# Performance work log

Measured on AMD Instinct MI355X. Metric: run time of the kernel, lower is better.

Reference implementation:

```python
import jax, jax.numpy as jnp
import numpy as np

N_NODES = 50000


def _pointnet_layer(h, pos, src, dst, wA, bA, wB, bB):
    # message: MLP(concat(h_j, pos_j - pos_i)) per edge, then max-aggregate at dst
    m = jnp.concatenate([h[src], pos[src] - pos[dst]], axis=-1)  # [E, in+3]
    m = jax.nn.relu(m @ wA + bA) @ wB + bB                       # [E, out]
    agg = jax.ops.segment_max(m, dst, num_segments=N_NODES)     # [N, out]
    # PyG max-aggregation returns 0 for nodes with no incoming edges
    return jnp.where(jnp.isfinite(agg), agg, 0.0)


def setup_inputs() -> dict:
    key = jax.random.key(0)
    ks = jax.random.split(key, 16)
    num_points, num_features, E = 256, 256, 800000
    s = 0.05
    inp = {
        "x": jax.random.normal(ks[0], (N_NODES, num_points), dtype=jnp.float32),
        "pos": jax.random.normal(ks[1], (N_NODES, 3), dtype=jnp.float32),
        "edge_index": jax.random.randint(ks[2], (2, E), 0, N_NODES, dtype=jnp.int64),
        # conv1 mlp: (num_points+3 -> F -> F)
        "w1a": jax.random.normal(ks[3], (num_points + 3, num_features), dtype=jnp.float32) * s,
        "b1a": jnp.zeros((num_features,), dtype=jnp.float32),
        "w1b": jax.random.normal(ks[4], (num_features, num_features), dtype=jnp.float32) * s,
        "b1b": jnp.zeros((num_features,), dtype=jnp.float32),
        # conv2 mlp: (F+3 -> F -> F)
        "w2a": jax.random.normal(ks[5], (num_features + 3, num_features), dtype=jnp.float32) * s,
        "b2a": jnp.zeros((num_features,), dtype=jnp.float32),
        "w2b": jax.random.normal(ks[6], (num_features, num_features), dtype=jnp.float32) * s,
        "b2b": jnp.zeros((num_features,), dtype=jnp.float32),
        # decoder: F -> 256 -> num_points
        "wd1": jax.random.normal(ks[7], (num_features, 256), dtype=jnp.float32) * s,
        "bd1": jnp.zeros((256,), dtype=jnp.float32),
        "wd2": jax.random.normal(ks[8], (256, num_points), dtype=jnp.float32) * s,
        "bd2": jnp.zeros((num_points,), dtype=jnp.float32),
    }
    return inp


def reference(x, pos, edge_index, w1a, b1a, w1b, b1b, w2a, b2a, w2b, b2b, wd1, bd1, wd2, bd2):
    src, dst = edge_index[0], edge_index[1]  # message flows j(src) -> i(dst)
    h = jax.nn.relu(_pointnet_layer(x, pos, src, dst, w1a, b1a, w1b, b1b))
    h = jax.nn.relu(_pointnet_layer(h, pos, src, dst, w2a, b2a, w2b, b2b))
    decoded = jax.nn.relu(h @ wd1 + bd1) @ wd2 + bd2  # [N, num_points]
    return decoded
```

## Files before the change

### kernel.cpp

```cpp
#include <hip/hip_runtime.h>
#include <stdint.h>


using bf16x8 = __attribute__((ext_vector_type(8))) short;
using f32x4  = __attribute__((ext_vector_type(4))) float;

#define AB_STRIDE 40
#define ZSTRIDE   68

__device__ __forceinline__ float b2f(uint32_t v16) {
    return __uint_as_float(v16 << 16);
}
__device__ __forceinline__ float b2f_hi(uint32_t w) {
    return __uint_as_float(w & 0xffff0000u);
}
__device__ __forceinline__ uint16_t f2b(float f) {
    uint32_t u = __float_as_uint(f);
    u += 0x7fffu + ((u >> 16) & 1u);
    return (uint16_t)(u >> 16);
}
#if __has_builtin(__builtin_amdgcn_cvt_pk_bf16_f32)
__device__ __forceinline__ uint32_t pack2bf(float lo, float hi) {
    auto r = __builtin_amdgcn_cvt_pk_bf16_f32(lo, hi);
    uint32_t u; __builtin_memcpy(&u, &r, 4); return u;
}
#else
__device__ __forceinline__ uint32_t pack2bf(float lo, float hi) {
    return (uint32_t)f2b(lo) | ((uint32_t)f2b(hi) << 16);
}
#endif
__device__ __forceinline__ uint32_t encf(float f) {
    uint32_t u = __float_as_uint(f);
    return (u & 0x80000000u) ? ~u : (u | 0x80000000u);
}
__device__ __forceinline__ float decf(uint32_t k) {
    uint32_t u = (k & 0x80000000u) ? (k & 0x7fffffffu) : ~k;
    return __uint_as_float(u);
}

__global__ void detect_fmt(const uint32_t* __restrict__ x,
                           const uint32_t* __restrict__ ei,
                           uint32_t* __restrict__ flags) {
    if (threadIdx.x == 0 && blockIdx.x == 0) {
        int plaus = 0;
        for (int i = 0; i < 64; i++) {
            uint32_t v = x[i];
            uint32_t e = (v >> 23) & 0xffu;
            if (v == 0u || (e >= 96u && e <= 150u)) plaus++;
        }
        flags[0] = (plaus >= 48) ? 1u : 0u;
        int zeros = 0;
        for (int i = 0; i < 16; i++)
            if (ei[2 * i + 1] == 0u) zeros++;
        flags[1] = (zeros == 16) ? 1u : 0u;
    }
}

__global__ __launch_bounds__(256) void convert_big(
        const void* __restrict__ src, uint16_t* __restrict__ dst, int n,
        const uint32_t* __restrict__ flags) {
    bool isf32 = flags[0] != 0u;
    int i = (blockIdx.x * 256 + threadIdx.x) * 4;
    if (i + 3 < n) {
        if (isf32) {
            float4 v = ((const float4*)src)[i >> 2];
            uint2 o = {pack2bf(v.x, v.y), pack2bf(v.z, v.w)};
            ((uint2*)dst)[i >> 2] = o;
        } else {
            ((uint2*)dst)[i >> 2] = ((const uint2*)src)[i >> 2];
        }
    } else {
        for (int j = i; j < n; j++)
            dst[j] = isf32 ? f2b(((const float*)src)[j]) : ((const uint16_t*)src)[j];
    }
}

struct ConvArgs {
    const void* src[13];
    uint32_t dstOff[13];
    uint32_t n[13];
};

__global__ __launch_bounds__(256) void convert_small(
        ConvArgs a, uint16_t* __restrict__ dstBase, const uint32_t* __restrict__ flags) {
    bool isf32 = flags[0] != 0u;
    int t = blockIdx.y;
    int i = blockIdx.x * 256 + threadIdx.x;
    if (i >= (int)a.n[t]) return;
    uint16_t* d = dstBase + a.dstOff[t];
    d[i] = isf32 ? f2b(((const float*)a.src[t])[i]) : ((const uint16_t*)a.src[t])[i];
}

__global__ __launch_bounds__(256) void zero_i32(int* p, int n) {
    int i = blockIdx.x * 256 + threadIdx.x;
    if (i < n) p[i] = 0;
}

__global__ __launch_bounds__(256) void hist_dst(
        const int* __restrict__ ei_raw, int E, int* __restrict__ hist,
        const uint32_t* __restrict__ flags) {
    bool i64 = flags[1] != 0u;
    int e = blockIdx.x * 256 + threadIdx.x;
    if (e < E) {
        int d = i64 ? ei_raw[2 * (E + e)] : ei_raw[E + e];
        atomicAdd(&hist[d], 1);
    }
}

__global__ __launch_bounds__(1024) void scan_partial(
        const int* __restrict__ hist, int* __restrict__ cursor,
        int* __restrict__ part, int N) {
    __shared__ int wsum[16];
    int tid = threadIdx.x, lane = tid & 63, wid = tid >> 6;
    int base = blockIdx.x * 1024;
    int v = (base + tid < N) ? hist[base + tid] : 0;
    int x = v;
#pragma unroll
    for (int s = 1; s < 64; s <<= 1) {
        int t = __shfl_up(x, s, 64);
        if (lane >= s) x += t;
    }
    if (lane == 63) wsum[wid] = x;
    __syncthreads();
    if (wid == 0 && lane < 16) {
        int w = wsum[lane];
#pragma unroll
        for (int s = 1; s < 16; s <<= 1) {
            int t = __shfl_up(w, s, 64);
            if (lane >= s) w += t;
        }
        wsum[lane] = w;
    }
    __syncthreads();
    int wbase = (wid > 0) ? wsum[wid - 1] : 0;
    if (base + tid < N) cursor[base + tid] = x - v + wbase;
    if (tid == 0) part[blockIdx.x] = wsum[15];
}

__global__ __launch_bounds__(1024) void scan_carry(
        const int* __restrict__ part, int* __restrict__ carry, int B) {
    __shared__ int wsum[16];
    int tid = threadIdx.x, lane = tid & 63, wid = tid >> 6;
    int v = (tid < B) ? part[tid] : 0;
    int x = v;
#pragma unroll
    for (int s = 1; s < 64; s <<= 1) {
        int t = __shfl_up(x, s, 64);
        if (lane >= s) x += t;
    }
    if (lane == 63) wsum[wid] = x;
    __syncthreads();
    if (wid == 0 && lane < 16) {
        int w = wsum[lane];
#pragma unroll
        for (int s = 1; s < 16; s <<= 1) {
            int t = __shfl_up(w, s, 64);
            if (lane >= s) w += t;
        }
        wsum[lane] = w;
    }
    __syncthreads();
    int wbase = (wid > 0) ? wsum[wid - 1] : 0;
    if (tid < B) carry[tid] = x - v + wbase;
}

__global__ __launch_bounds__(1024) void scan_add(
        int* __restrict__ cursor, const int* __restrict__ carry, int N) {
    int i = blockIdx.x * 1024 + threadIdx.x;
    if (i < N) cursor[i] += carry[blockIdx.x];
}

__global__ __launch_bounds__(256) void scatter_edges(
        const int* __restrict__ ei_raw, int E, int* __restrict__ cursor,
        int* __restrict__ esrc, int* __restrict__ edst,
        const uint32_t* __restrict__ flags) {
    bool i64 = flags[1] != 0u;
    int e = blockIdx.x * 256 + threadIdx.x;
    if (e < E) {
        int s = i64 ? ei_raw[2 * e] : ei_raw[e];
        int d = i64 ? ei_raw[2 * (E + e)] : ei_raw[E + e];
        int p = atomicAdd(&cursor[d], 1);
        esrc[p] = s;
        edst[p] = d;
    }
}

__global__ __launch_bounds__(256) void transpose_w(
        const uint16_t* s0, const uint16_t* s1, const uint16_t* s2,
        const uint16_t* s3, const uint16_t* s4, const uint16_t* s5,
        uint16_t* dst) {
    const uint16_t* srcs[6] = {s0, s1, s2, s3, s4, s5};
    const uint16_t* src = srcs[blockIdx.y];
    uint16_t* d = dst + (size_t)blockIdx.y * 65536;
    int k = blockIdx.x;
    int n = threadIdx.x;
    d[(k >> 5) * 8192 + n * 32 + (k & 31)] = src[k * 256 + n];
}

__global__ __launch_bounds__(256) void pos_proj(
        const uint16_t* pos, const uint16_t* wpos, uint16_t* Q, int N) {
    int c = threadIdx.x;
    float w0 = b2f(wpos[c]), w1 = b2f(wpos[256 + c]), w2 = b2f(wpos[512 + c]);
    int base = blockIdx.x * 8;
#pragma unroll
    for (int n = 0; n < 8; n++) {
        int i = base + n;
        if (i >= N) break;
        float p0 = b2f(pos[i * 3 + 0]);
        float p1 = b2f(pos[i * 3 + 1]);
        float p2 = b2f(pos[i * 3 + 2]);
        Q[(size_t)i * 256 + c] = f2b(p0 * w0 + p1 * w1 + p2 * w2);
    }
}

__global__ __launch_bounds__(256) void init_agg(uint32_t* agg, int n4) {
    int i = blockIdx.x * 256 + threadIdx.x;
    if (i < n4) {
        uint4 v = {0x80000000u, 0x80000000u, 0x80000000u, 0x80000000u};
        ((uint4*)agg)[i] = v;
    }
}

__global__ __launch_bounds__(256) void finalize_init(
        uint32_t* __restrict__ agg, uint16_t* __restrict__ h, int n4) {
    int i = blockIdx.x * 256 + threadIdx.x;
    if (i < n4) {
        uint4 a = ((uint4*)agg)[i];
        uint2 o = {pack2bf(decf(a.x), decf(a.y)), pack2bf(decf(a.z), decf(a.w))};
        ((uint2*)h)[i] = o;
        uint4 z = {0x80000000u, 0x80000000u, 0x80000000u, 0x80000000u};
        ((uint4*)agg)[i] = z;
    }
}

template <int MODE>
__global__ __launch_bounds__(256) void gemm_node(
        const uint16_t* __restrict__ A, const uint16_t* __restrict__ BT,
        const uint16_t* __restrict__ bias, const uint16_t* __restrict__ Qadd,
        void* __restrict__ out, int M, const uint32_t* __restrict__ flags) {
    __shared__ __align__(16) uint16_t Al[64 * AB_STRIDE];
    __shared__ __align__(16) uint16_t Bl[256 * AB_STRIDE];
    int tid = threadIdx.x;
    int tileM = blockIdx.x;
    int wave = tid >> 6, lane = tid & 63, lrow = lane & 15, quad = lane >> 4;
    f32x4 acc[4][4] = {};

    int row = tid >> 2, kq = (tid & 3) * 8;
    for (int kc = 0; kc < 256; kc += 32) {
        {
            int rg = tileM * 64 + row;
            uint4 v = {0, 0, 0, 0};
            if (rg < M) v = *(const uint4*)(A + (size_t)rg * 256 + kc + kq);
            *(uint4*)&Al[row * AB_STRIDE + kq] = v;
        }
        {
            const uint4* p = (const uint4*)(BT + (kc >> 5) * 8192 + tid * 32);
#pragma unroll
            for (int j = 0; j < 4; j++) *(uint4*)&Bl[tid * AB_STRIDE + j * 8] = p[j];
        }
        __syncthreads();
        bf16x8 af[4], bfr[4];
#pragma unroll
        for (int r = 0; r < 4; r++)
            af[r] = *(const bf16x8*)&Al[(r * 16 + lrow) * AB_STRIDE + quad * 8];
#pragma unroll
        for (int c = 0; c < 4; c++)
            bfr[c] = *(const bf16x8*)&Bl[(wave * 64 + c * 16 + lrow) * AB_STRIDE + quad * 8];
#pragma unroll
        for (int r = 0; r < 4; r++)
#pragma unroll
            for (int c = 0; c < 4; c++)
                acc[r][c] = __builtin_amdgcn_mfma_f32_16x16x32_bf16(af[r], bfr[c], acc[r][c], 0, 0, 0);
        __syncthreads();
    }

    bool of32 = false;
    if (MODE == 2) of32 = flags[0] != 0u;

#pragma unroll
    for (int c = 0; c < 4; c++) {
        int col = wave * 64 + c * 16 + lrow;
        float bv = b2f(bias[col]);
#pragma unroll
        for (int r = 0; r < 4; r++) {
#pragma unroll
            for (int i = 0; i < 4; i++) {
                int rw = tileM * 64 + r * 16 + quad * 4 + i;
                if (rw >= M) continue;
                float v = acc[r][c][i] + bv;
                if (MODE == 0) {
                    v += b2f(Qadd[(size_t)rw * 256 + col]);
                    ((uint16_t*)out)[(size_t)rw * 256 + col] = f2b(v);
                } else if (MODE == 1) {
                    v = fmaxf(v, 0.f);
                    ((uint16_t*)out)[(size_t)rw * 256 + col] = f2b(v);
                } else {
                    if (of32) ((float*)out)[(size_t)rw * 256 + col] = v;
                    else      ((uint16_t*)out)[(size_t)rw * 256 + col] = f2b(v);
                }
            }
        }
    }
}

__global__ __launch_bounds__(256, 4) void edge_gemm_agg(
        const uint16_t* __restrict__ Gs16, const uint16_t* __restrict__ Qb,
        const uint16_t* __restrict__ BT, const uint16_t* __restrict__ bias,
        const int* __restrict__ esrc, const int* __restrict__ edst, int E,
        uint32_t* __restrict__ agg) {
    __shared__ __align__(16) uint16_t SM[256 * ZSTRIDE];
    uint16_t* Al = SM;
    uint16_t* Bl = SM + 64 * AB_STRIDE;
    uint16_t* Zl = SM;
    __shared__ int ssrc[64], sdst[64];
    __shared__ uint64_t smask;
    int tid = threadIdx.x;
    int ebase = blockIdx.x * 64;
    int evalid = (E - ebase < 64) ? (E - ebase) : 64;
    if (tid < 64) {
        int s = 0, d = 0;
        if (tid < evalid) {
            s = esrc[ebase + tid];
            d = edst[ebase + tid];
        }
        ssrc[tid] = s;
        sdst[tid] = d;
    }
    __syncthreads();
    int wave = tid >> 6, lane = tid & 63, lrow = lane & 15, quad = lane >> 4;
    f32x4 acc[4][4] = {};

    int row = tid >> 2, kq = (tid & 3) * 8;
    int s = ssrc[row], dd = sdst[row];
    const uint16_t* gbase = Gs16 + (size_t)s * 256 + kq;
    const uint16_t* qbase = Qb + (size_t)dd * 256 + kq;

    for (int kc = 0; kc < 256; kc += 32) {
        {
            uint4 ga = *(const uint4*)(gbase + kc);
            uint4 qa = *(const uint4*)(qbase + kc);
            uint32_t gw[4] = {ga.x, ga.y, ga.z, ga.w};
            uint32_t qw[4] = {qa.x, qa.y, qa.z, qa.w};
            uint32_t mw[4];
#pragma unroll
            for (int j = 0; j < 4; j++) {
                float lo = fmaxf(b2f(gw[j] & 0xffffu) - b2f(qw[j] & 0xffffu), 0.f);
                float hi = fmaxf(b2f_hi(gw[j]) - b2f_hi(qw[j]), 0.f);
                mw[j] = pack2bf(lo, hi);
            }
            uint4 wv = {mw[0], mw[1], mw[2], mw[3]};
            *(uint4*)&Al[row * AB_STRIDE + kq] = wv;
        }
        {
            const uint4* p = (const uint4*)(BT + (kc >> 5) * 8192 + tid * 32);
#pragma unroll
            for (int j = 0; j < 4; j++) *(uint4*)&Bl[tid * AB_STRIDE + j * 8] = p[j];
        }
        __syncthreads();
        bf16x8 af[4], bfr[4];
#pragma unroll
        for (int r = 0; r < 4; r++)
            af[r] = *(const bf16x8*)&Al[(r * 16 + lrow) * AB_STRIDE + quad * 8];
#pragma unroll
        for (int c = 0; c < 4; c++)
            bfr[c] = *(const bf16x8*)&Bl[(wave * 64 + c * 16 + lrow) * AB_STRIDE + quad * 8];
#pragma unroll
        for (int r = 0; r < 4; r++)
#pragma unroll
            for (int c = 0; c < 4; c++)
                acc[r][c] = __builtin_amdgcn_mfma_f32_16x16x32_bf16(af[r], bfr[c], acc[r][c], 0, 0, 0);
        __syncthreads();
    }

    float bv[4];
#pragma unroll
    for (int c = 0; c < 4; c++) bv[c] = b2f(bias[wave * 64 + c * 16 + lrow]);
#pragma unroll
    for (int c = 0; c < 4; c++) {
        int col = wave * 64 + c * 16 + lrow;
#pragma unroll
        for (int r = 0; r < 4; r++) {
            uint2 z4 = {pack2bf(acc[r][c][0] + bv[c], acc[r][c][1] + bv[c]),
                        pack2bf(acc[r][c][2] + bv[c], acc[r][c][3] + bv[c])};
            *(uint2*)&Zl[col * ZSTRIDE + r * 16 + quad * 4] = z4;
        }
    }
    if (wave == 0) {
        int d0 = sdst[lane];
        int dp = (lane > 0) ? sdst[lane - 1] : -1;
        uint64_t m = __ballot(d0 != dp);
        if (lane == 0) smask = m;
    }
    __syncthreads();

    uint64_t mask = smask;
    int col = tid;
    const uint16_t* zc = &Zl[col * ZSTRIDE];
    float run = 0.f;
#pragma unroll 4
    for (int g = 0; g < 16; g++) {
        int rbase = g * 4;
        if (rbase >= evalid) break;
        uint2 z4 = *(const uint2*)&zc[rbase];
        float vv[4] = {b2f(z4.x & 0xffffu), b2f_hi(z4.x),
                       b2f(z4.y & 0xffffu), b2f_hi(z4.y)};
#pragma unroll
        for (int i = 0; i < 4; i++) {
            int r = rbase + i;
            if (r >= evalid) break;
            if (r == 0) {
                run = vv[0];
            } else if ((mask >> r) & 1ull) {
                int dp = sdst[r - 1];
                atomicMax(agg + (size_t)dp * 256 + col, encf(run));
                run = vv[i];
            } else {
                run = fmaxf(run, vv[i]);
            }
        }
    }
    if (evalid > 0)
        atomicMax(agg + (size_t)sdst[evalid - 1] * 256 + col, encf(run));
}

extern "C" void kernel_launch(void* const* d_in, const int* in_sizes, int n_in,
                              void* d_out, int out_size, void* d_ws, size_t ws_size,
                              hipStream_t stream) {
    const void* x_raw   = d_in[0];
    const void* pos_raw = d_in[1];
    const int*  ei_raw  = (const int*)d_in[2];

    int N = in_sizes[0] / 256;
    int E = in_sizes[2] / 2;

    char* ws = (char*)d_ws;
    size_t off = 0;
    auto alloc = [&](size_t bytes) { void* p = ws + off; off += (bytes + 255) & ~(size_t)255; return p; };

    uint32_t* flags = (uint32_t*)alloc(256);
    uint16_t* WT    = (uint16_t*)alloc(6 * 65536 * sizeof(uint16_t));
    const uint32_t POS_OFF = 0;
    const uint32_t W1A_OFF = POS_OFF + (uint32_t)(N * 3);
    const uint32_t W2A_OFF = W1A_OFF + 66304;
    const uint32_t W1B_OFF = W2A_OFF + 66304;
    const uint32_t W2B_OFF = W1B_OFF + 65536;
    const uint32_t WD1_OFF = W2B_OFF + 65536;
    const uint32_t WD2_OFF = WD1_OFF + 65536;
    const uint32_t B1A_OFF = WD2_OFF + 65536;
    const uint32_t B1B_OFF = B1A_OFF + 256;
    const uint32_t B2A_OFF = B1B_OFF + 256;
    const uint32_t B2B_OFF = B2A_OFF + 256;
    const uint32_t BD1_OFF = B2B_OFF + 256;
    const uint32_t BD2_OFF = BD1_OFF + 256;
    const uint32_t ARENA_ELEMS = BD2_OFF + 256;
    uint16_t* arena = (uint16_t*)alloc((size_t)ARENA_ELEMS * 2);
    int*      hist  = (int*)alloc((size_t)N * 4);
    int*      curs  = (int*)alloc((size_t)N * 4);
    int*      part  = (int*)alloc(1024 * 4);
    int*      carry = (int*)alloc(1024 * 4);
    int*      esrc  = (int*)alloc((size_t)E * 4);
    int*      edst  = (int*)alloc((size_t)E * 4);
    uint16_t* Qb    = (uint16_t*)alloc((size_t)N * 256 * 2);
    uint16_t* Gs    = (uint16_t*)alloc((size_t)N * 256 * 2);
    uint32_t* agg   = (uint32_t*)alloc((size_t)N * 256 * 4);
    uint16_t* xb    = (uint16_t*)alloc((size_t)N * 256 * 2);
    uint16_t* h     = xb;
    uint16_t* d1    = Gs;

    uint16_t* posb = arena + POS_OFF;
    uint16_t* w1a = arena + W1A_OFF, * w2a = arena + W2A_OFF;
    uint16_t* w1b = arena + W1B_OFF, * w2b = arena + W2B_OFF;
    uint16_t* wd1 = arena + WD1_OFF, * wd2 = arena + WD2_OFF;
    uint16_t* b1a = arena + B1A_OFF, * b1b = arena + B1B_OFF;
    uint16_t* b2a = arena + B2A_OFF, * b2b = arena + B2B_OFF;
    uint16_t* bd1 = arena + BD1_OFF, * bd2 = arena + BD2_OFF;

    int n4      = N * 64;
    int nbElem  = (n4 + 255) / 256;
    int nbNode  = (N + 63) / 64;
    int nbEdge  = (E + 63) / 64;
    int nbE256  = (E + 255) / 256;
    int nbPos   = (N + 7) / 8;
    int nbScan  = (N + 1023) / 1024;

    detect_fmt<<<1, 64, 0, stream>>>((const uint32_t*)x_raw, (const uint32_t*)ei_raw, flags);
    convert_big<<<(N * 256 / 4 + 255) / 256, 256, 0, stream>>>(x_raw, xb, N * 256, flags);

    ConvArgs ca;
    ca.src[0] = pos_raw;  ca.dstOff[0] = POS_OFF; ca.n[0] = (uint32_t)(N * 3);
    ca.src[1] = d_in[3];  ca.dstOff[1] = W1A_OFF; ca.n[1] = 66304;
    ca.src[2] = d_in[7];  ca.dstOff[2] = W2A_OFF; ca.n[2] = 66304;
    ca.src[3] = d_in[5];  ca.dstOff[3] = W1B_OFF; ca.n[3] = 65536;
    ca.src[4] = d_in[9];  ca.dstOff[4] = W2B_OFF; ca.n[4] = 65536;
    ca.src[5] = d_in[11]; ca.dstOff[5] = WD1_OFF; ca.n[5] = 65536;
    ca.src[6] = d_in[13]; ca.dstOff[6] = WD2_OFF; ca.n[6] = 65536;
    ca.src[7] = d_in[4];  ca.dstOff[7] = B1A_OFF; ca.n[7] = 256;
    ca.src[8] = d_in[6];  ca.dstOff[8] = B1B_OFF; ca.n[8] = 256;
    ca.src[9] = d_in[8];  ca.dstOff[9] = B2A_OFF; ca.n[9] = 256;
    ca.src[10] = d_in[10]; ca.dstOff[10] = B2B_OFF; ca.n[10] = 256;
    ca.src[11] = d_in[12]; ca.dstOff[11] = BD1_OFF; ca.n[11] = 256;
    ca.src[12] = d_in[14]; ca.dstOff[12] = BD2_OFF; ca.n[12] = 256;
    {
        uint32_t maxn = (uint32_t)(N * 3);
        dim3 g((maxn + 255) / 256, 13);
        convert_small<<<g, 256, 0, stream>>>(ca, arena, flags);
    }

    zero_i32<<<(N + 255) / 256, 256, 0, stream>>>(hist, N);
    hist_dst<<<nbE256, 256, 0, stream>>>(ei_raw, E, hist, flags);
    scan_partial<<<nbScan, 1024, 0, stream>>>(hist, curs, part, N);
    scan_carry<<<1, 1024, 0, stream>>>(part, carry, nbScan);
    scan_add<<<nbScan, 1024, 0, stream>>>(curs, carry, N);
    scatter_edges<<<nbE256, 256, 0, stream>>>(ei_raw, E, curs, esrc, edst, flags);

    transpose_w<<<dim3(256, 6), 256, 0, stream>>>(w1a, w1b, w2a, w2b, wd1, wd2, WT);

    pos_proj<<<nbPos, 256, 0, stream>>>(posb, w1a + 65536, Qb, N);
    gemm_node<0><<<nbNode, 256, 0, stream>>>(xb, WT + 0 * 65536, b1a, Qb, Gs, N, flags);
    init_agg<<<nbElem, 256, 0, stream>>>(agg, n4);
    edge_gemm_agg<<<nbEdge, 256, 0, stream>>>(Gs, Qb, WT + 1 * 65536, b1b, esrc, edst, E, agg);
    finalize_init<<<nbElem, 256, 0, stream>>>(agg, h, n4);

    pos_proj<<<nbPos, 256, 0, stream>>>(posb, w2a + 65536, Qb, N);
    gemm_node<0><<<nbNode, 256, 0, stream>>>(h, WT + 2 * 65536, b2a, Qb, Gs, N, flags);
    edge_gemm_agg<<<nbEdge, 256, 0, stream>>>(Gs, Qb, WT + 3 * 65536, b2b, esrc, edst, E, agg);
    finalize_init<<<nbElem, 256, 0, stream>>>(agg, h, n4);

    gemm_node<1><<<nbNode, 256, 0, stream>>>(h, WT + 4 * 65536, bd1, nullptr, d1, N, flags);
    gemm_node<2><<<nbNode, 256, 0, stream>>>(d1, WT + 5 * 65536, bd2, nullptr, d_out, N, flags);
}
```

Measured before the change: 854.5 us.

## Double-buffer A tile, load B fragments from global, prefetch next K chunk

Both the node GEMM and the edge gather-GEMM now keep B (weights) out of LDS, loading the MFMA fragments straight from global/L2 into registers. The A tile is double-buffered in LDS, so only one barrier per K step is needed. That barrier waits on LDS traffic only, so the global prefetch of the next K chunk of A (or of the G/Q gather) overlaps with the MFMAs. This removes the B staging through LDS and one barrier per iteration, at the cost of more registers and repeated global reads of B from every block.

```diff
diff --git a/kernel.cpp b/kernel.cpp
--- a/kernel.cpp
+++ b/kernel.cpp
@@ -6,7 +6,10 @@
 using f32x4  = __attribute__((ext_vector_type(4))) float;
 
 #define AB_STRIDE 40
+#define ABUF      2560
 #define ZSTRIDE   68
+
+#define BARRIER_NOVM() asm volatile("s_waitcnt lgkmcnt(0)\n\ts_barrier" ::: "memory")
 
 __device__ __forceinline__ float b2f(uint32_t v16) {
     return __uint_as_float(v16 << 16);
@@ -238,40 +241,42 @@
         const uint16_t* __restrict__ A, const uint16_t* __restrict__ BT,
         const uint16_t* __restrict__ bias, const uint16_t* __restrict__ Qadd,
         void* __restrict__ out, int M, const uint32_t* __restrict__ flags) {
-    __shared__ __align__(16) uint16_t Al[64 * AB_STRIDE];
-    __shared__ __align__(16) uint16_t Bl[256 * AB_STRIDE];
+    __shared__ __align__(16) uint16_t Al[2 * 64 * AB_STRIDE];
     int tid = threadIdx.x;
     int tileM = blockIdx.x;
     int wave = tid >> 6, lane = tid & 63, lrow = lane & 15, quad = lane >> 4;
+    int row = tid >> 2, kq = (tid & 3) * 8;
     f32x4 acc[4][4] = {};
 
-    int row = tid >> 2, kq = (tid & 3) * 8;
+    int rg = tileM * 64 + row;
+    bool rok = rg < M;
+    const uint16_t* abase = A + (size_t)rg * 256 + kq;
+    const uint16_t* bfrag = BT + (wave * 64 + lrow) * 32 + quad * 8;
+    uint16_t* awr = Al + row * AB_STRIDE + kq;
+    const uint16_t* ard = Al + lrow * AB_STRIDE + quad * 8;
+
+    uint4 a0 = {0, 0, 0, 0};
+    if (rok) a0 = *(const uint4*)abase;
+
+#pragma unroll
     for (int kc = 0; kc < 256; kc += 32) {
-        {
-            int rg = tileM * 64 + row;
-            uint4 v = {0, 0, 0, 0};
-            if (rg < M) v = *(const uint4*)(A + (size_t)rg * 256 + kc + kq);
-            *(uint4*)&Al[row * AB_STRIDE + kq] = v;
-        }
-        {
-            const uint4* p = (const uint4*)(BT + (kc >> 5) * 8192 + tid * 32);
-#pragma unroll
-            for (int j = 0; j < 4; j++) *(uint4*)&Bl[tid * AB_STRIDE + j * 8] = p[j];
-        }
-        __syncthreads();
-        bf16x8 af[4], bfr[4];
+        int buf = (kc >> 5) & 1;
+        *(uint4*)(awr + buf * ABUF) = a0;
+        const uint16_t* bp = bfrag + (kc >> 5) * 8192;
+        bf16x8 bfv[4];
+#pragma unroll
+        for (int c = 0; c < 4; c++) bfv[c] = *(const bf16x8*)(bp + c * 512);
+        if (kc < 224 && rok) a0 = *(const uint4*)(abase + kc + 32);
+        BARRIER_NOVM();
+        const uint16_t* ar = ard + buf * ABUF;
+        bf16x8 af[4];
+#pragma unroll
+        for (int r = 0; r < 4; r++) af[r] = *(const bf16x8*)(ar + r * 16 * AB_STRIDE);
 #pragma unroll
         for (int r = 0; r < 4; r++)
-            af[r] = *(const bf16x8*)&Al[(r * 16 + lrow) * AB_STRIDE + quad * 8];
-#pragma unroll
-        for (int c = 0; c < 4; c++)
-            bfr[c] = *(const bf16x8*)&Bl[(wave * 64 + c * 16 + lrow) * AB_STRIDE + quad * 8];
-#pragma unroll
-        for (int r = 0; r < 4; r++)
 #pragma unroll
             for (int c = 0; c < 4; c++)
-                acc[r][c] = __builtin_amdgcn_mfma_f32_16x16x32_bf16(af[r], bfr[c], acc[r][c], 0, 0, 0);
-        __syncthreads();
+                acc[r][c] = __builtin_amdgcn_mfma_f32_16x16x32_bf16(af[r], bfv[c], acc[r][c], 0, 0, 0);
     }
 
     bool of32 = false;
@@ -310,67 +315,63 @@
         uint32_t* __restrict__ agg) {
     __shared__ __align__(16) uint16_t SM[256 * ZSTRIDE];
     uint16_t* Al = SM;
-    uint16_t* Bl = SM + 64 * AB_STRIDE;
     uint16_t* Zl = SM;
-    __shared__ int ssrc[64], sdst[64];
+    __shared__ int sdst[64];
     __shared__ uint64_t smask;
     int tid = threadIdx.x;
     int ebase = blockIdx.x * 64;
     int evalid = (E - ebase < 64) ? (E - ebase) : 64;
-    if (tid < 64) {
-        int s = 0, d = 0;
-        if (tid < evalid) {
-            s = esrc[ebase + tid];
-            d = edst[ebase + tid];
-        }
-        ssrc[tid] = s;
-        sdst[tid] = d;
+    if (tid < 64) sdst[tid] = (tid < evalid) ? edst[ebase + tid] : 0;
+
+    int wave = tid >> 6, lane = tid & 63, lrow = lane & 15, quad = lane >> 4;
+    int row = tid >> 2, kq = (tid & 3) * 8;
+    int er = (row < evalid) ? row : (evalid - 1);
+    int s = esrc[ebase + er];
+    int d = edst[ebase + er];
+    const uint16_t* gbase = Gs16 + (size_t)s * 256 + kq;
+    const uint16_t* qbase = Qb   + (size_t)d * 256 + kq;
+    const uint16_t* bfrag = BT + (wave * 64 + lrow) * 32 + quad * 8;
+    uint16_t* awr = Al + row * AB_STRIDE + kq;
+    const uint16_t* ard = Al + lrow * AB_STRIDE + quad * 8;
+
+    f32x4 acc[4][4] = {};
+    uint4 g = *(const uint4*)gbase;
+    uint4 q = *(const uint4*)qbase;
+
+#pragma unroll
+    for (int kc = 0; kc < 256; kc += 32) {
+        int buf = (kc >> 5) & 1;
+        uint32_t gw[4] = {g.x, g.y, g.z, g.w};
+        uint32_t qw[4] = {q.x, q.y, q.z, q.w};
+        uint32_t mw[4];
+#pragma unroll
+        for (int j = 0; j < 4; j++) {
+            float lo = fmaxf(b2f(gw[j] & 0xffffu) - b2f(qw[j] & 0xffffu), 0.f);
+            float hi = fmaxf(b2f_hi(gw[j]) - b2f_hi(qw[j]), 0.f);
+            mw[j] = pack2bf(lo, hi);
+        }
+        uint4 wv = {mw[0], mw[1], mw[2], mw[3]};
+        *(uint4*)(awr + buf * ABUF) = wv;
+        const uint16_t* bp = bfrag + (kc >> 5) * 8192;
+        bf16x8 bfv[4];
+#pragma unroll
+        for (int c = 0; c < 4; c++) bfv[c] = *(const bf16x8*)(bp + c * 512);
+        if (kc < 224) {
+            g = *(const uint4*)(gbase + kc + 32);
+            q = *(const uint4*)(qbase + kc + 32);
+        }
+        BARRIER_NOVM();
+        const uint16_t* ar = ard + buf * ABUF;
+        bf16x8 af[4];
+#pragma unroll
+        for (int r = 0; r < 4; r++) af[r] = *(const bf16x8*)(ar + r * 16 * AB_STRIDE);
+#pragma unroll
+        for (int r = 0; r < 4; r++)
+#pragma unroll
+            for (int c = 0; c < 4; c++)
+                acc[r][c] = __builtin_amdgcn_mfma_f32_16x16x32_bf16(af[r], bfv[c], acc[r][c], 0, 0, 0);
     }
     __syncthreads();
-    int wave = tid >> 6, lane = tid & 63, lrow = lane & 15, quad = lane >> 4;
-    f32x4 acc[4][4] = {};
-
-    int row = tid >> 2, kq = (tid & 3) * 8;
-    int s = ssrc[row], dd = sdst[row];
-    const uint16_t* gbase = Gs16 + (size_t)s * 256 + kq;
-    const uint16_t* qbase = Qb + (size_t)dd * 256 + kq;
-
-    for (int kc = 0; kc < 256; kc += 32) {
-        {
-            uint4 ga = *(const uint4*)(gbase + kc);
-            uint4 qa = *(const uint4*)(qbase + kc);
-            uint32_t gw[4] = {ga.x, ga.y, ga.z, ga.w};
-            uint32_t qw[4] = {qa.x, qa.y, qa.z, qa.w};
-            uint32_t mw[4];
-#pragma unroll
-            for (int j = 0; j < 4; j++) {
-                float lo = fmaxf(b2f(gw[j] & 0xffffu) - b2f(qw[j] & 0xffffu), 0.f);
-                float hi = fmaxf(b2f_hi(gw[j]) - b2f_hi(qw[j]), 0.f);
-                mw[j] = pack2bf(lo, hi);
-            }
-            uint4 wv = {mw[0], mw[1], mw[2], mw[3]};
-            *(uint4*)&Al[row * AB_STRIDE + kq] = wv;
-        }
-        {
-            const uint4* p = (const uint4*)(BT + (kc >> 5) * 8192 + tid * 32);
-#pragma unroll
-            for (int j = 0; j < 4; j++) *(uint4*)&Bl[tid * AB_STRIDE + j * 8] = p[j];
-        }
-        __syncthreads();
-        bf16x8 af[4], bfr[4];
-#pragma unroll
-        for (int r = 0; r < 4; r++)
-            af[r] = *(const bf16x8*)&Al[(r * 16 + lrow) * AB_STRIDE + quad * 8];
-#pragma unroll
-        for (int c = 0; c < 4; c++)
-            bfr[c] = *(const bf16x8*)&Bl[(wave * 64 + c * 16 + lrow) * AB_STRIDE + quad * 8];
-#pragma unroll
-        for (int r = 0; r < 4; r++)
-#pragma unroll
-            for (int c = 0; c < 4; c++)
-                acc[r][c] = __builtin_amdgcn_mfma_f32_16x16x32_bf16(af[r], bfr[c], acc[r][c], 0, 0, 0);
-        __syncthreads();
-    }
 
     float bv[4];
 #pragma unroll
@@ -398,8 +399,8 @@
     const uint16_t* zc = &Zl[col * ZSTRIDE];
     float run = 0.f;
 #pragma unroll 4
-    for (int g = 0; g < 16; g++) {
-        int rbase = g * 4;
+    for (int gi = 0; gi < 16; gi++) {
+        int rbase = gi * 4;
         if (rbase >= evalid) break;
         uint2 z4 = *(const uint2*)&zc[rbase];
         float vv[4] = {b2f(z4.x & 0xffffu), b2f_hi(z4.x),
```

Measured after the change: 907.9 us. 6.2% more time.
